# Kernel tuning notes

Hardware: AMD Instinct MI355X
Metric: run time of the kernel (lower is better)

## Reference

```python
import jax, jax.numpy as jnp
import numpy as np

EMB = 1024
N_HEAD = 16
D_K = EMB // N_HEAD


def setup_inputs() -> dict:
    key = jax.random.key(0)
    ks = jax.random.split(key, 11)
    B, S = 4, 2048
    scale = 1.0 / np.sqrt(EMB)
    inp = {
        "q": jax.random.normal(ks[0], (B, S, EMB), jnp.float32),
        "k": jax.random.normal(ks[1], (B, S, EMB), jnp.float32),
        "v": jax.random.normal(ks[2], (B, S, EMB), jnp.float32),
        "Wq": jax.random.normal(ks[3], (EMB, EMB), jnp.float32) * scale,
        "bq": jnp.zeros((EMB,), jnp.float32),
        "Wk": jax.random.normal(ks[4], (EMB, EMB), jnp.float32) * scale,
        "bk": jnp.zeros((EMB,), jnp.float32),
        "Wv": jax.random.normal(ks[5], (EMB, EMB), jnp.float32) * scale,
        "bv": jnp.zeros((EMB,), jnp.float32),
        "Wo": jax.random.normal(ks[6], (EMB, EMB), jnp.float32) * scale,
        "bo": jnp.zeros((EMB,), jnp.float32),
    }
    return inp


def reference(q, k, v, Wq, bq, Wk, bk, Wv, bv, Wo, bo):
    B, S, _ = q.shape
    # project and split heads: [B, H, S, d_k]
    def split(x, W, b):
        y = x @ W.T + b
        return y.reshape(B, -1, N_HEAD, D_K).transpose(0, 2, 1, 3)

    qh = split(q, Wq, bq)
    kh = split(k, Wk, bk)
    vh = split(v, Wv, bv)
    scores = jnp.einsum("bhqd,bhkd->bhqk", qh, kh) / jnp.sqrt(
        jnp.asarray(D_K, qh.dtype))
    attn = jax.nn.softmax(scores, axis=-1)
    out = jnp.einsum("bhqk,bhkd->bhqd", attn, vh)
    out = out.transpose(0, 2, 1, 3).reshape(B, -1, EMB)
    return out @ Wo.T + bo
```

## Files before the change

### kernel.cpp

```cpp
#include <hip/hip_runtime.h>
#include <hip/hip_bf16.h>

#define S_LEN 2048
#define EMB_D 1024
#define NH 16
#define DK 64
#define BATCH 4

typedef __attribute__((ext_vector_type(8))) short short8;
typedef __attribute__((ext_vector_type(4))) float f32x4;
typedef __attribute__((ext_vector_type(8))) unsigned short ushort8;
typedef __attribute__((ext_vector_type(4))) unsigned short ushort4v;
typedef __attribute__((ext_vector_type(4))) unsigned int uint4v;
typedef __attribute__((ext_vector_type(2))) unsigned int uint2v;

__device__ inline unsigned short f2bf(float x) {
    unsigned u = __builtin_bit_cast(unsigned, x);
    u = (u + 0x7fffu + ((u >> 16) & 1u)) >> 16;
    return (unsigned short)u;
}

__device__ inline unsigned cvtpk(float lo, float hi) {
    unsigned r;
    asm("v_cvt_pk_bf16_f32 %0, %1, %2" : "=v"(r) : "v"(lo), "v"(hi));
    return r;
}

typedef const __attribute__((address_space(1))) unsigned int* gas_p;
typedef __attribute__((address_space(3))) unsigned int* las_p;
__device__ inline void gload16(const void* g, void* l) {
    __builtin_amdgcn_global_load_lds((gas_p)g, (las_p)l, 16, 0, 0);
}

struct CvtArgs {
    const float* src[7];
    unsigned short* dst[7];
    int starts[8];
    int ntens;
};

__global__ __launch_bounds__(256) void cvt_all(CvtArgs a) {
    int b = blockIdx.x;
    int t = 0;
#pragma unroll
    for (int i = 1; i < 7; ++i)
        if (i < a.ntens && b >= a.starts[i]) t = i;
    int rel = b - a.starts[t];
    size_t i = (size_t)rel * 2048 + (size_t)threadIdx.x * 8;
    float4 x = *(const float4*)&a.src[t][i];
    float4 y = *(const float4*)&a.src[t][i + 4];
    uint4v w;
    w.x = cvtpk(x.x, x.y); w.y = cvtpk(x.z, x.w);
    w.z = cvtpk(y.x, y.y); w.w = cvtpk(y.z, y.w);
    *(uint4v*)&a.dst[t][i] = w;
}

__global__ __launch_bounds__(256) void gemm_qkv(
    const unsigned short* __restrict__ Aq, const unsigned short* __restrict__ Ak,
    const unsigned short* __restrict__ Av, const unsigned short* __restrict__ Wcat,
    const float* __restrict__ bq, const float* __restrict__ bk, const float* __restrict__ bv,
    unsigned short* __restrict__ Qh, unsigned short* __restrict__ Kh,
    unsigned short* __restrict__ Vt, float qscale)
{
    const int K = EMB_D;
    __shared__ unsigned short As[2][128][64];
    __shared__ unsigned short Bs[2][128][64];

    const int tid = threadIdx.x;
    const int lane = tid & 63;
    const int wid = tid >> 6;
    const int wr = wid >> 1, wc = wid & 1;
    const int l15 = lane & 15, l4 = lane >> 4;
    const int lx7 = l15 & 7;

    const int bid = blockIdx.x;
    const int xcd = bid & 7, j = bid >> 3;
    const int tau = j >> 6, jj = j & 63;
    const int bnl = jj & 7;
    const int bm = xcd * 8 + (jj >> 3);

    const unsigned short* Ab = tau == 0 ? Aq : (tau == 1 ? Ak : Av);
    const unsigned short* Bw = Wcat + (size_t)tau * EMB_D * EMB_D;
    const float* bias = tau == 0 ? bq : (tau == 1 ? bk : bv);
    const float osc = tau == 0 ? qscale : 1.0f;

    const int srow = lane >> 3;
    const int sgl = lane & 7;

    f32x4 acc[4][4];
#pragma unroll
    for (int m = 0; m < 4; ++m)
#pragma unroll
        for (int n = 0; n < 4; ++n) {
            f32x4 z = {0.f, 0.f, 0.f, 0.f};
            acc[m][n] = z;
        }

    auto stageB = [&](int c, int kt) {
#pragma unroll
        for (int q2 = 0; q2 < 4; ++q2) {
            int r = wid * 32 + q2 * 8 + srow;
            gload16(&Bw[(size_t)(bnl * 128 + r) * K + kt * 64 + (sgl ^ srow) * 8],
                    &Bs[c][wid * 32 + q2 * 8][0]);
        }
    };
    auto stageA = [&](int c, int kt) {
#pragma unroll
        for (int q2 = 0; q2 < 4; ++q2) {
            int r = wid * 32 + q2 * 8 + srow;
            gload16(&Ab[(size_t)(bm * 128 + r) * K + kt * 64 + (sgl ^ srow) * 8],
                    &As[c][wid * 32 + q2 * 8][0]);
        }
    };

    stageA(0, 0);
    stageB(0, 0);
    __syncthreads();

    for (int kt = 0; kt < K / 64; ++kt) {
        const int c = kt & 1;
        if (kt + 1 < K / 64) {
            stageA(c ^ 1, kt + 1);
            stageB(c ^ 1, kt + 1);
        }
#pragma unroll
        for (int h = 0; h < 2; ++h) {
            short8 af[4], bf[4];
#pragma unroll
            for (int m = 0; m < 4; ++m)
                af[m] = *(const short8*)&As[c][wr * 64 + m * 16 + l15][((h * 4 + l4) ^ lx7) * 8];
#pragma unroll
            for (int n = 0; n < 4; ++n)
                bf[n] = *(const short8*)&Bs[c][wc * 64 + n * 16 + l15][((h * 4 + l4) ^ lx7) * 8];
#pragma unroll
            for (int m = 0; m < 4; ++m)
#pragma unroll
                for (int n = 0; n < 4; ++n)
                    acc[m][n] = __builtin_amdgcn_mfma_f32_16x16x32_bf16(af[m], bf[n], acc[m][n], 0, 0, 0);
        }
        __syncthreads();
    }

#pragma unroll
    for (int m = 0; m < 4; ++m) {
#pragma unroll
        for (int n = 0; n < 4; ++n) {
            int gm0 = bm * 128 + wr * 64 + m * 16 + l4 * 4;
            int gn = bnl * 128 + wc * 64 + n * 16 + l15;
            if (tau == 2) {
                int b = gm0 >> 11, s0 = gm0 & 2047;
                int h = gn >> 6, d = gn & 63;
                ushort4v w;
#pragma unroll
                for (int r = 0; r < 4; ++r)
                    w[r] = f2bf(acc[m][n][r] + bias[gn]);
                *(ushort4v*)&Vt[((size_t)(b * NH + h) * DK + d) * S_LEN + s0] = w;
            } else {
                unsigned short* Out = tau == 0 ? Qh : Kh;
#pragma unroll
                for (int r = 0; r < 4; ++r) {
                    int gm = gm0 + r;
                    float val = (acc[m][n][r] + bias[gn]) * osc;
                    int b = gm >> 11, s = gm & 2047;
                    int h = gn >> 6, d = gn & 63;
                    Out[((size_t)(b * NH + h) * S_LEN + s) * DK + d] = f2bf(val);
                }
            }
        }
    }
}

template<int A_MODE, int OUT_MODE>
__global__ __launch_bounds__(256) void gemm_bt(
    const void* __restrict__ Aptr, const unsigned short* __restrict__ Bw,
    const float* __restrict__ bias, void* __restrict__ Cout, float oscale)
{
    const int K = EMB_D;
    __shared__ unsigned short As[2][128][64];
    __shared__ unsigned short Bs[2][128][64];

    const int tid = threadIdx.x;
    const int lane = tid & 63;
    const int wid = tid >> 6;
    const int wr = wid >> 1, wc = wid & 1;
    const int l15 = lane & 15, l4 = lane >> 4;
    const int lx7 = l15 & 7;

    const int bid = blockIdx.x;
    const int bm = (bid & 7) * 8 + (bid >> 6);
    const int bn = (bid >> 3) & 7;

    const int srow = lane >> 3;
    const int sgl = lane & 7;

    const float* Af = (const float*)Aptr;
    const unsigned short* Ab = (const unsigned short*)Aptr;

    f32x4 acc[4][4];
#pragma unroll
    for (int m = 0; m < 4; ++m)
#pragma unroll
        for (int n = 0; n < 4; ++n) {
            f32x4 z = {0.f, 0.f, 0.f, 0.f};
            acc[m][n] = z;
        }

    float4 areg[8];

    auto stageB = [&](int c, int kt) {
#pragma unroll
        for (int q2 = 0; q2 < 4; ++q2) {
            int r = wid * 32 + q2 * 8 + srow;
            gload16(&Bw[(size_t)(bn * 128 + r) * K + kt * 64 + (sgl ^ srow) * 8],
                    &Bs[c][wid * 32 + q2 * 8][0]);
        }
    };
    auto stageA1 = [&](int c, int kt) {
#pragma unroll
        for (int q2 = 0; q2 < 4; ++q2) {
            int r = wid * 32 + q2 * 8 + srow;
            gload16(&Ab[(size_t)(bm * 128 + r) * K + kt * 64 + (sgl ^ srow) * 8],
                    &As[c][wid * 32 + q2 * 8][0]);
        }
    };
    auto loadA0 = [&](int kt) {
#pragma unroll
        for (int j = 0; j < 8; ++j) {
            int f = tid + j * 256;
            int r = f >> 4, c4 = f & 15;
            areg[j] = *(const float4*)&Af[(size_t)(bm * 128 + r) * K + kt * 64 + c4 * 4];
        }
    };
    auto writeA0 = [&](int c) {
#pragma unroll
        for (int j = 0; j < 8; ++j) {
            int f = tid + j * 256;
            int r = f >> 4, c4 = f & 15;
            uint2v w;
            w.x = cvtpk(areg[j].x, areg[j].y);
            w.y = cvtpk(areg[j].z, areg[j].w);
            int col = (((c4 >> 1) ^ (r & 7)) << 3) + ((c4 & 1) << 2);
            *(uint2v*)&As[c][r][col] = w;
        }
    };

    if (A_MODE == 0) loadA0(0); else stageA1(0, 0);
    stageB(0, 0);
    if (A_MODE == 0) {
        asm volatile("s_waitcnt vmcnt(0)" ::: "memory");
        writeA0(0);
    }
    __syncthreads();

    for (int kt = 0; kt < K / 64; ++kt) {
        const int c = kt & 1;
        const bool pf = (kt + 1 < K / 64);
        if (pf) {
            if (A_MODE == 0) loadA0(kt + 1); else stageA1(c ^ 1, kt + 1);
            stageB(c ^ 1, kt + 1);
        }
#pragma unroll
        for (int h = 0; h < 2; ++h) {
            short8 af[4], bf[4];
#pragma unroll
            for (int m = 0; m < 4; ++m)
                af[m] = *(const short8*)&As[c][wr * 64 + m * 16 + l15][((h * 4 + l4) ^ lx7) * 8];
#pragma unroll
            for (int n = 0; n < 4; ++n)
                bf[n] = *(const short8*)&Bs[c][wc * 64 + n * 16 + l15][((h * 4 + l4) ^ lx7) * 8];
#pragma unroll
            for (int m = 0; m < 4; ++m)
#pragma unroll
                for (int n = 0; n < 4; ++n)
                    acc[m][n] = __builtin_amdgcn_mfma_f32_16x16x32_bf16(af[m], bf[n], acc[m][n], 0, 0, 0);
        }
        if (pf && A_MODE == 0) {
            asm volatile("s_waitcnt vmcnt(0)" ::: "memory");
            writeA0(c ^ 1);
        }
        __syncthreads();
    }

#pragma unroll
    for (int m = 0; m < 4; ++m) {
#pragma unroll
        for (int n = 0; n < 4; ++n) {
            int gm0 = bm * 128 + wr * 64 + m * 16 + l4 * 4;
            int gn = bn * 128 + wc * 64 + n * 16 + l15;
            if (OUT_MODE == 2) {
                int b = gm0 >> 11, s0 = gm0 & 2047;
                int h = gn >> 6, d = gn & 63;
                ushort4v w;
#pragma unroll
                for (int r = 0; r < 4; ++r)
                    w[r] = f2bf((acc[m][n][r] + bias[gn]) * oscale);
                *(ushort4v*)&((unsigned short*)Cout)[((size_t)(b * NH + h) * DK + d) * S_LEN + s0] = w;
            } else {
#pragma unroll
                for (int r = 0; r < 4; ++r) {
                    int gm = gm0 + r;
                    float val = (acc[m][n][r] + bias[gn]) * oscale;
                    if (OUT_MODE == 1) {
                        int b = gm >> 11, s = gm & 2047;
                        int h = gn >> 6, d = gn & 63;
                        ((unsigned short*)Cout)[((size_t)(b * NH + h) * S_LEN + s) * DK + d] = f2bf(val);
                    } else {
                        ((float*)Cout)[(size_t)gm * EMB_D + gn] = val;
                    }
                }
            }
        }
    }
}

__global__ __launch_bounds__(256, 4) void attn_fwd(
    const unsigned short* __restrict__ Qh, const unsigned short* __restrict__ Kh,
    const unsigned short* __restrict__ Vt, unsigned short* __restrict__ Aout)
{
    __shared__ unsigned short Ks[2][64][64];
    __shared__ unsigned short Vts[2][64][64];

    const int tid = threadIdx.x;
    const int lane = tid & 63;
    const int wid = tid >> 6;
    const int l15 = lane & 15, l4 = lane >> 4;
    const int lx7 = l15 & 7;

    const int bid = blockIdx.x;
    const int swz = (bid & 7) * 128 + (bid >> 3);
    const int bh = swz >> 4, qt = swz & 15;

    const unsigned short* Qb = Qh + (size_t)bh * S_LEN * DK;
    const unsigned short* Kb = Kh + (size_t)bh * S_LEN * DK;
    const unsigned short* Vtb = Vt + (size_t)bh * DK * S_LEN;

    const int srow = lane >> 3;
    const int sgl = lane & 7;

    auto stage = [&](int c, int kt) {
#pragma unroll
        for (int q2 = 0; q2 < 2; ++q2) {
            int q = wid * 2 + q2;
            int rho = q * 8 + srow;
            int kappa = ((rho >> 5) & 1) * 32 + ((rho >> 3) & 1) * 16 +
                        ((rho >> 2) & 1) * 8 + ((rho >> 4) & 1) * 4 + (rho & 3);
            gload16(&Kb[(size_t)(kt * 64 + kappa) * DK + (sgl ^ srow) * 8],
                    &Ks[c][q * 8][0]);
            gload16(&Vtb[(size_t)rho * S_LEN + kt * 64 + (sgl ^ srow) * 8],
                    &Vts[c][q * 8][0]);
        }
    };

    short8 qf[2][2];
#pragma unroll
    for (int m = 0; m < 2; ++m) {
        int qrow = qt * 128 + wid * 32 + m * 16 + l15;
#pragma unroll
        for (int h = 0; h < 2; ++h)
            qf[m][h] = *(const short8*)&Qb[(size_t)qrow * DK + h * 32 + l4 * 8];
    }

    f32x4 ot[2][5];
#pragma unroll
    for (int m = 0; m < 2; ++m)
#pragma unroll
        for (int n = 0; n < 5; ++n) {
            f32x4 z = {0.f, 0.f, 0.f, 0.f};
            ot[m][n] = z;
        }

    short8 ones;
#pragma unroll
    for (int e = 0; e < 8; ++e) ones[e] = (short)0x3F80;

    stage(0, 0);
    __syncthreads();

    for (int kt = 0; kt < S_LEN / 64; ++kt) {
        const int c = kt & 1;
        if (kt + 1 < S_LEN / 64) stage(c ^ 1, kt + 1);

        f32x4 st[2][4];
#pragma unroll
        for (int m = 0; m < 2; ++m)
#pragma unroll
            for (int kb = 0; kb < 4; ++kb) {
                f32x4 z = {0.f, 0.f, 0.f, 0.f};
                st[m][kb] = z;
            }
        __builtin_amdgcn_s_setprio(1);
#pragma unroll
        for (int h = 0; h < 2; ++h)
#pragma unroll
            for (int kb = 0; kb < 4; ++kb) {
                short8 kf = *(const short8*)&Ks[c][kb * 16 + l15][((h * 4 + l4) ^ lx7) * 8];
#pragma unroll
                for (int m = 0; m < 2; ++m)
                    st[m][kb] = __builtin_amdgcn_mfma_f32_16x16x32_bf16(kf, qf[m][h], st[m][kb], 0, 0, 0);
            }
        __builtin_amdgcn_s_setprio(0);

        short8 pa[2][2];
#pragma unroll
        for (int m = 0; m < 2; ++m) {
#pragma unroll
            for (int kb = 0; kb < 4; ++kb)
#pragma unroll
                for (int r = 0; r < 4; ++r)
                    st[m][kb][r] = __builtin_amdgcn_exp2f(st[m][kb][r]);
#pragma unroll
            for (int h = 0; h < 2; ++h) {
                uint4v w;
                w.x = cvtpk(st[m][2 * h][0], st[m][2 * h][1]);
                w.y = cvtpk(st[m][2 * h][2], st[m][2 * h][3]);
                w.z = cvtpk(st[m][2 * h + 1][0], st[m][2 * h + 1][1]);
                w.w = cvtpk(st[m][2 * h + 1][2], st[m][2 * h + 1][3]);
                pa[m][h] = __builtin_bit_cast(short8, w);
            }
        }

        __builtin_amdgcn_s_setprio(1);
#pragma unroll
        for (int n = 0; n < 4; ++n)
#pragma unroll
            for (int h = 0; h < 2; ++h) {
                short8 vb = *(const short8*)&Vts[c][n * 16 + l15][((h * 4 + l4) ^ lx7) * 8];
#pragma unroll
                for (int m = 0; m < 2; ++m)
                    ot[m][n] = __builtin_amdgcn_mfma_f32_16x16x32_bf16(pa[m][h], vb, ot[m][n], 0, 0, 0);
            }
#pragma unroll
        for (int h = 0; h < 2; ++h)
#pragma unroll
            for (int m = 0; m < 2; ++m)
                ot[m][4] = __builtin_amdgcn_mfma_f32_16x16x32_bf16(pa[m][h], ones, ot[m][4], 0, 0, 0);
        __builtin_amdgcn_s_setprio(0);
        __syncthreads();
    }

    const int b = bh >> 4, hh = bh & 15;
#pragma unroll
    for (int m = 0; m < 2; ++m) {
#pragma unroll
        for (int r = 0; r < 4; ++r) {
            float inv = 1.0f / ot[m][4][r];
            int s = qt * 128 + wid * 32 + m * 16 + l4 * 4 + r;
#pragma unroll
            for (int n = 0; n < 4; ++n) {
                int d = n * 16 + l15;
                Aout[((size_t)(b * S_LEN + s)) * EMB_D + hh * DK + d] = f2bf(ot[m][n][r] * inv);
            }
        }
    }
}

extern "C" void kernel_launch(void* const* d_in, const int* in_sizes, int n_in,
                              void* d_out, int out_size, void* d_ws, size_t ws_size,
                              hipStream_t stream) {
    const float* q  = (const float*)d_in[0];
    const float* k  = (const float*)d_in[1];
    const float* v  = (const float*)d_in[2];
    const float* Wq = (const float*)d_in[3];
    const float* bq = (const float*)d_in[4];
    const float* Wk = (const float*)d_in[5];
    const float* bk = (const float*)d_in[6];
    const float* Wv = (const float*)d_in[7];
    const float* bv = (const float*)d_in[8];
    const float* Wo = (const float*)d_in[9];
    const float* bo = (const float*)d_in[10];

    const size_t seg = (size_t)BATCH * NH * S_LEN * DK;
    const size_t wseg = (size_t)EMB_D * EMB_D;
    unsigned short* Qh = (unsigned short*)d_ws;
    unsigned short* Kh = Qh + seg;
    unsigned short* Vh = Kh + seg;
    unsigned short* Ao = Vh + seg;
    unsigned short* Wqb = Ao + seg;
    unsigned short* Wkb = Wqb + wseg;
    unsigned short* Wvb = Wkb + wseg;
    unsigned short* Wob = Wvb + wseg;
    unsigned short* qb = Wob + wseg;
    unsigned short* kb2 = qb + seg;
    unsigned short* vb2 = kb2 + seg;

    const size_t full_elems = seg * 7 + wseg * 4;
    const bool full = ws_size >= full_elems * 2;

    const float qscale = 0.18033688011112042f;

    const int WBLK = (int)(wseg / 2048);
    const int SBLK = (int)(seg / 2048);

    CvtArgs ca;
    ca.src[0] = Wq;  ca.dst[0] = Wqb;
    ca.src[1] = Wk;  ca.dst[1] = Wkb;
    ca.src[2] = Wv;  ca.dst[2] = Wvb;
    ca.src[3] = Wo;  ca.dst[3] = Wob;
    ca.starts[0] = 0;
    ca.starts[1] = WBLK;
    ca.starts[2] = WBLK * 2;
    ca.starts[3] = WBLK * 3;
    int nb = WBLK * 4;
    if (full) {
        ca.src[4] = q; ca.dst[4] = qb;
        ca.src[5] = k; ca.dst[5] = kb2;
        ca.src[6] = v; ca.dst[6] = vb2;
        ca.starts[4] = nb;
        ca.starts[5] = nb + SBLK;
        ca.starts[6] = nb + SBLK * 2;
        ca.ntens = 7;
        nb += SBLK * 3;
    } else {
        ca.src[4] = ca.src[5] = ca.src[6] = Wq;
        ca.dst[4] = ca.dst[5] = ca.dst[6] = Wqb;
        ca.starts[4] = ca.starts[5] = ca.starts[6] = nb;
        ca.ntens = 4;
    }
    ca.starts[7] = nb;
    cvt_all<<<nb, 256, 0, stream>>>(ca);

    if (full) {
        gemm_qkv<<<1536, 256, 0, stream>>>(qb, kb2, vb2, Wqb, bq, bk, bv,
                                           Qh, Kh, Vh, qscale);
    } else {
        gemm_bt<0, 1><<<512, 256, 0, stream>>>((const void*)q, Wqb, bq, (void*)Qh, qscale);
        gemm_bt<0, 1><<<512, 256, 0, stream>>>((const void*)k, Wkb, bk, (void*)Kh, 1.0f);
        gemm_bt<0, 2><<<512, 256, 0, stream>>>((const void*)v, Wvb, bv, (void*)Vh, 1.0f);
    }

    attn_fwd<<<1024, 256, 0, stream>>>(Qh, Kh, Vh, Ao);

    gemm_bt<1, 0><<<512, 256, 0, stream>>>((const void*)Ao, Wob, bo, d_out, 1.0f);
}
```

Measured before the change: 195.1 us.

## Use triple-buffered K=32 pipeline for QKV and output projection GEMMs

Replaces the double-buffered K=64 LDS loop in the QKV projection GEMM with a three-stage K=32 pipeline that prefetches two tiles ahead, using explicit vmcnt waits and raw barriers with sched_barrier fences. A new XOR swizzle fits the narrower tiles. The output projection now uses a dedicated kernel with the same loop instead of the generic gemm_bt, assuming Ao is bf16. The aim is to hide global-load latency better; the cost is twice as many barriers per K and correctness that depends on the hand-written waitcnt counts.

```diff
diff --git a/kernel.cpp b/kernel.cpp
--- a/kernel.cpp
+++ b/kernel.cpp
@@ -55,7 +55,51 @@
     *(uint4v*)&a.dst[t][i] = w;
 }
 
-__global__ __launch_bounds__(256) void gemm_qkv(
+
+#define GEMM32_LOOP(AB_EXPR, BW_EXPR)                                              \
+    auto stage = [&](int s, int kt) {                                              \
+        _Pragma("unroll")                                                          \
+        for (int j2 = 0; j2 < 2; ++j2) {                                           \
+            int rb = j2 * 64 + w16;                                                \
+            gload16(AB_EXPR, &As[s][rb][0]);                                       \
+        }                                                                          \
+        _Pragma("unroll")                                                          \
+        for (int j2 = 0; j2 < 2; ++j2) {                                           \
+            int rb = j2 * 64 + w16;                                                \
+            gload16(BW_EXPR, &Bs[s][rb][0]);                                       \
+        }                                                                          \
+    };                                                                             \
+    stage(0, 0);                                                                   \
+    stage(1, 1);                                                                   \
+    asm volatile("s_waitcnt vmcnt(4)" ::: "memory");                               \
+    __builtin_amdgcn_sched_barrier(0);                                             \
+    __builtin_amdgcn_s_barrier();                                                  \
+    __builtin_amdgcn_sched_barrier(0);                                             \
+    for (int kt = 0; kt < 32; ++kt) {                                              \
+        const int scur = kt % 3;                                                   \
+        if (kt + 2 < 32) stage((kt + 2) % 3, kt + 2);                              \
+        __builtin_amdgcn_sched_barrier(0);                                         \
+        short8 af[4], bf[4];                                                       \
+        _Pragma("unroll")                                                          \
+        for (int m = 0; m < 4; ++m)                                                \
+            af[m] = *(const short8*)&As[scur][wr * 64 + m * 16 + l15][fsl];        \
+        _Pragma("unroll")                                                          \
+        for (int n = 0; n < 4; ++n)                                                \
+            bf[n] = *(const short8*)&Bs[scur][wc * 64 + n * 16 + l15][fsl];        \
+        _Pragma("unroll")                                                          \
+        for (int m = 0; m < 4; ++m)                                                \
+            _Pragma("unroll")                                                      \
+            for (int n = 0; n < 4; ++n)                                            \
+                acc[m][n] = __builtin_amdgcn_mfma_f32_16x16x32_bf16(               \
+                    af[m], bf[n], acc[m][n], 0, 0, 0);                             \
+        if (kt + 2 < 32) { asm volatile("s_waitcnt vmcnt(4)" ::: "memory"); }      \
+        else             { asm volatile("s_waitcnt vmcnt(0)" ::: "memory"); }      \
+        __builtin_amdgcn_sched_barrier(0);                                         \
+        __builtin_amdgcn_s_barrier();                                              \
+        __builtin_amdgcn_sched_barrier(0);                                         \
+    }
+
+__global__ __launch_bounds__(256) void gemm_qkv32(
     const unsigned short* __restrict__ Aq, const unsigned short* __restrict__ Ak,
     const unsigned short* __restrict__ Av, const unsigned short* __restrict__ Wcat,
     const float* __restrict__ bq, const float* __restrict__ bk, const float* __restrict__ bv,
@@ -63,15 +107,14 @@
     unsigned short* __restrict__ Vt, float qscale)
 {
     const int K = EMB_D;
-    __shared__ unsigned short As[2][128][64];
-    __shared__ unsigned short Bs[2][128][64];
+    __shared__ unsigned short As[3][128][32];
+    __shared__ unsigned short Bs[3][128][32];
 
     const int tid = threadIdx.x;
     const int lane = tid & 63;
     const int wid = tid >> 6;
     const int wr = wid >> 1, wc = wid & 1;
     const int l15 = lane & 15, l4 = lane >> 4;
-    const int lx7 = l15 & 7;
 
     const int bid = blockIdx.x;
     const int xcd = bid & 7, j = bid >> 3;
@@ -80,12 +123,14 @@
     const int bm = xcd * 8 + (jj >> 3);
 
     const unsigned short* Ab = tau == 0 ? Aq : (tau == 1 ? Ak : Av);
-    const unsigned short* Bw = Wcat + (size_t)tau * EMB_D * EMB_D;
+    const unsigned short* Bw = Wcat + (size_t)tau * (size_t)EMB_D * EMB_D;
     const float* bias = tau == 0 ? bq : (tau == 1 ? bk : bv);
     const float osc = tau == 0 ? qscale : 1.0f;
 
-    const int srow = lane >> 3;
-    const int sgl = lane & 7;
+    const int srow4 = lane >> 2;
+    const int sgl4 = ((lane & 3) ^ ((lane >> 3) & 3)) * 8;
+    const int w16 = wid * 16;
+    const int fsl = (l4 ^ ((l15 >> 1) & 3)) * 8;
 
     f32x4 acc[4][4];
 #pragma unroll
@@ -96,50 +141,9 @@
             acc[m][n] = z;
         }
 
-    auto stageB = [&](int c, int kt) {
-#pragma unroll
-        for (int q2 = 0; q2 < 4; ++q2) {
-            int r = wid * 32 + q2 * 8 + srow;
-            gload16(&Bw[(size_t)(bnl * 128 + r) * K + kt * 64 + (sgl ^ srow) * 8],
-                    &Bs[c][wid * 32 + q2 * 8][0]);
-        }
-    };
-    auto stageA = [&](int c, int kt) {
-#pragma unroll
-        for (int q2 = 0; q2 < 4; ++q2) {
-            int r = wid * 32 + q2 * 8 + srow;
-            gload16(&Ab[(size_t)(bm * 128 + r) * K + kt * 64 + (sgl ^ srow) * 8],
-                    &As[c][wid * 32 + q2 * 8][0]);
-        }
-    };
-
-    stageA(0, 0);
-    stageB(0, 0);
-    __syncthreads();
-
-    for (int kt = 0; kt < K / 64; ++kt) {
-        const int c = kt & 1;
-        if (kt + 1 < K / 64) {
-            stageA(c ^ 1, kt + 1);
-            stageB(c ^ 1, kt + 1);
-        }
-#pragma unroll
-        for (int h = 0; h < 2; ++h) {
-            short8 af[4], bf[4];
-#pragma unroll
-            for (int m = 0; m < 4; ++m)
-                af[m] = *(const short8*)&As[c][wr * 64 + m * 16 + l15][((h * 4 + l4) ^ lx7) * 8];
-#pragma unroll
-            for (int n = 0; n < 4; ++n)
-                bf[n] = *(const short8*)&Bs[c][wc * 64 + n * 16 + l15][((h * 4 + l4) ^ lx7) * 8];
-#pragma unroll
-            for (int m = 0; m < 4; ++m)
-#pragma unroll
-                for (int n = 0; n < 4; ++n)
-                    acc[m][n] = __builtin_amdgcn_mfma_f32_16x16x32_bf16(af[m], bf[n], acc[m][n], 0, 0, 0);
-        }
-        __syncthreads();
-    }
+    GEMM32_LOOP(
+        &Ab[(size_t)(bm * 128 + rb + srow4) * K + kt * 32 + sgl4],
+        &Bw[(size_t)(bnl * 128 + rb + srow4) * K + kt * 32 + sgl4])
 
 #pragma unroll
     for (int m = 0; m < 4; ++m) {
@@ -166,6 +170,58 @@
                     Out[((size_t)(b * NH + h) * S_LEN + s) * DK + d] = f2bf(val);
                 }
             }
+        }
+    }
+}
+
+__global__ __launch_bounds__(256) void gemm32_f32out(
+    const unsigned short* __restrict__ Ain, const unsigned short* __restrict__ Bwp,
+    const float* __restrict__ bias, float* __restrict__ Cout)
+{
+    const int K = EMB_D;
+    __shared__ unsigned short As[3][128][32];
+    __shared__ unsigned short Bs[3][128][32];
+
+    const int tid = threadIdx.x;
+    const int lane = tid & 63;
+    const int wid = tid >> 6;
+    const int wr = wid >> 1, wc = wid & 1;
+    const int l15 = lane & 15, l4 = lane >> 4;
+
+    const int bid = blockIdx.x;
+    const int bm = (bid & 7) * 8 + (bid >> 6);
+    const int bn = (bid >> 3) & 7;
+
+    const unsigned short* Ab = Ain;
+    const unsigned short* Bw = Bwp;
+
+    const int srow4 = lane >> 2;
+    const int sgl4 = ((lane & 3) ^ ((lane >> 3) & 3)) * 8;
+    const int w16 = wid * 16;
+    const int fsl = (l4 ^ ((l15 >> 1) & 3)) * 8;
+
+    f32x4 acc[4][4];
+#pragma unroll
+    for (int m = 0; m < 4; ++m)
+#pragma unroll
+        for (int n = 0; n < 4; ++n) {
+            f32x4 z = {0.f, 0.f, 0.f, 0.f};
+            acc[m][n] = z;
+        }
+
+    GEMM32_LOOP(
+        &Ab[(size_t)(bm * 128 + rb + srow4) * K + kt * 32 + sgl4],
+        &Bw[(size_t)(bn * 128 + rb + srow4) * K + kt * 32 + sgl4])
+
+#pragma unroll
+    for (int m = 0; m < 4; ++m) {
+#pragma unroll
+        for (int n = 0; n < 4; ++n) {
+            int gm0 = bm * 128 + wr * 64 + m * 16 + l4 * 4;
+            int gn = bn * 128 + wc * 64 + n * 16 + l15;
+#pragma unroll
+            for (int r = 0; r < 4; ++r)
+                Cout[(size_t)(gm0 + r) * EMB_D + gn] = acc[m][n][r] + bias[gn];
         }
     }
 }
@@ -520,8 +576,8 @@
     cvt_all<<<nb, 256, 0, stream>>>(ca);
 
     if (full) {
-        gemm_qkv<<<1536, 256, 0, stream>>>(qb, kb2, vb2, Wqb, bq, bk, bv,
-                                           Qh, Kh, Vh, qscale);
+        gemm_qkv32<<<1536, 256, 0, stream>>>(qb, kb2, vb2, Wqb, bq, bk, bv,
+                                             Qh, Kh, Vh, qscale);
     } else {
         gemm_bt<0, 1><<<512, 256, 0, stream>>>((const void*)q, Wqb, bq, (void*)Qh, qscale);
         gemm_bt<0, 1><<<512, 256, 0, stream>>>((const void*)k, Wkb, bk, (void*)Kh, 1.0f);
@@ -530,5 +586,5 @@
 
     attn_fwd<<<1024, 256, 0, stream>>>(Qh, Kh, Vh, Ao);
 
-    gemm_bt<1, 0><<<512, 256, 0, stream>>>((const void*)Ao, Wob, bo, d_out, 1.0f);
-}
+    gemm32_f32out<<<512, 256, 0, stream>>>(Ao, Wob, bo, (float*)d_out);
+}
```

Measured after the change: 205.6 us. 1.05x slower.

## Single-buffer GEMM LDS tiles for occupancy and add dedicated output-projection kernel

Applied to the files above, without the earlier changes.

The QKV projection GEMM drops its double-buffered LDS staging in favour of a single buffer with a sync after loading, and gains a launch-bounds hint of 4 blocks per CU. The point is to cut LDS and register use so more blocks can be resident and hide latency through occupancy rather than software prefetch. A new gemm_o kernel with the same single-buffer structure and an XCD-aware block mapping replaces the templated gemm_bt for the output projection. The cost is that global loads no longer overlap MFMA work inside a block, and there is an extra barrier every K step.

```diff
diff --git a/kernel.cpp b/kernel.cpp
--- a/kernel.cpp
+++ b/kernel.cpp
@@ -55,7 +55,7 @@
     *(uint4v*)&a.dst[t][i] = w;
 }
 
-__global__ __launch_bounds__(256) void gemm_qkv(
+__global__ __launch_bounds__(256, 4) void gemm_qkv(
     const unsigned short* __restrict__ Aq, const unsigned short* __restrict__ Ak,
     const unsigned short* __restrict__ Av, const unsigned short* __restrict__ Wcat,
     const float* __restrict__ bq, const float* __restrict__ bk, const float* __restrict__ bv,
@@ -63,8 +63,8 @@
     unsigned short* __restrict__ Vt, float qscale)
 {
     const int K = EMB_D;
-    __shared__ unsigned short As[2][128][64];
-    __shared__ unsigned short Bs[2][128][64];
+    __shared__ unsigned short As[128][64];
+    __shared__ unsigned short Bs[128][64];
 
     const int tid = threadIdx.x;
     const int lane = tid & 63;
@@ -80,7 +80,7 @@
     const int bm = xcd * 8 + (jj >> 3);
 
     const unsigned short* Ab = tau == 0 ? Aq : (tau == 1 ? Ak : Av);
-    const unsigned short* Bw = Wcat + (size_t)tau * EMB_D * EMB_D;
+    const unsigned short* Bw = Wcat + (size_t)tau * (size_t)EMB_D * EMB_D;
     const float* bias = tau == 0 ? bq : (tau == 1 ? bk : bv);
     const float osc = tau == 0 ? qscale : 1.0f;
 
@@ -96,42 +96,29 @@
             acc[m][n] = z;
         }
 
-    auto stageB = [&](int c, int kt) {
+    for (int kt = 0; kt < K / 64; ++kt) {
+#pragma unroll
+        for (int q2 = 0; q2 < 4; ++q2) {
+            int r = wid * 32 + q2 * 8 + srow;
+            gload16(&Ab[(size_t)(bm * 128 + r) * K + kt * 64 + (sgl ^ srow) * 8],
+                    &As[wid * 32 + q2 * 8][0]);
+        }
 #pragma unroll
         for (int q2 = 0; q2 < 4; ++q2) {
             int r = wid * 32 + q2 * 8 + srow;
             gload16(&Bw[(size_t)(bnl * 128 + r) * K + kt * 64 + (sgl ^ srow) * 8],
-                    &Bs[c][wid * 32 + q2 * 8][0]);
-        }
-    };
-    auto stageA = [&](int c, int kt) {
-#pragma unroll
-        for (int q2 = 0; q2 < 4; ++q2) {
-            int r = wid * 32 + q2 * 8 + srow;
-            gload16(&Ab[(size_t)(bm * 128 + r) * K + kt * 64 + (sgl ^ srow) * 8],
-                    &As[c][wid * 32 + q2 * 8][0]);
-        }
-    };
-
-    stageA(0, 0);
-    stageB(0, 0);
-    __syncthreads();
-
-    for (int kt = 0; kt < K / 64; ++kt) {
-        const int c = kt & 1;
-        if (kt + 1 < K / 64) {
-            stageA(c ^ 1, kt + 1);
-            stageB(c ^ 1, kt + 1);
-        }
+                    &Bs[wid * 32 + q2 * 8][0]);
+        }
+        __syncthreads();
 #pragma unroll
         for (int h = 0; h < 2; ++h) {
             short8 af[4], bf[4];
 #pragma unroll
             for (int m = 0; m < 4; ++m)
-                af[m] = *(const short8*)&As[c][wr * 64 + m * 16 + l15][((h * 4 + l4) ^ lx7) * 8];
+                af[m] = *(const short8*)&As[wr * 64 + m * 16 + l15][((h * 4 + l4) ^ lx7) * 8];
 #pragma unroll
             for (int n = 0; n < 4; ++n)
-                bf[n] = *(const short8*)&Bs[c][wc * 64 + n * 16 + l15][((h * 4 + l4) ^ lx7) * 8];
+                bf[n] = *(const short8*)&Bs[wc * 64 + n * 16 + l15][((h * 4 + l4) ^ lx7) * 8];
 #pragma unroll
             for (int m = 0; m < 4; ++m)
 #pragma unroll
@@ -166,6 +153,82 @@
                     Out[((size_t)(b * NH + h) * S_LEN + s) * DK + d] = f2bf(val);
                 }
             }
+        }
+    }
+}
+
+__global__ __launch_bounds__(256, 4) void gemm_o(
+    const unsigned short* __restrict__ Ain, const unsigned short* __restrict__ Bw,
+    const float* __restrict__ bias, float* __restrict__ Cout)
+{
+    const int K = EMB_D;
+    __shared__ unsigned short As[128][64];
+    __shared__ unsigned short Bs[128][64];
+
+    const int tid = threadIdx.x;
+    const int lane = tid & 63;
+    const int wid = tid >> 6;
+    const int wr = wid >> 1, wc = wid & 1;
+    const int l15 = lane & 15, l4 = lane >> 4;
+    const int lx7 = l15 & 7;
+
+    const int bid = blockIdx.x;
+    const int bm = (bid & 7) * 8 + (bid >> 6);
+    const int bn = (bid >> 3) & 7;
+
+    const int srow = lane >> 3;
+    const int sgl = lane & 7;
+
+    f32x4 acc[4][4];
+#pragma unroll
+    for (int m = 0; m < 4; ++m)
+#pragma unroll
+        for (int n = 0; n < 4; ++n) {
+            f32x4 z = {0.f, 0.f, 0.f, 0.f};
+            acc[m][n] = z;
+        }
+
+    for (int kt = 0; kt < K / 64; ++kt) {
+#pragma unroll
+        for (int q2 = 0; q2 < 4; ++q2) {
+            int r = wid * 32 + q2 * 8 + srow;
+            gload16(&Ain[(size_t)(bm * 128 + r) * K + kt * 64 + (sgl ^ srow) * 8],
+                    &As[wid * 32 + q2 * 8][0]);
+        }
+#pragma unroll
+        for (int q2 = 0; q2 < 4; ++q2) {
+            int r = wid * 32 + q2 * 8 + srow;
+            gload16(&Bw[(size_t)(bn * 128 + r) * K + kt * 64 + (sgl ^ srow) * 8],
+                    &Bs[wid * 32 + q2 * 8][0]);
+        }
+        __syncthreads();
+#pragma unroll
+        for (int h = 0; h < 2; ++h) {
+            short8 af[4], bf[4];
+#pragma unroll
+            for (int m = 0; m < 4; ++m)
+                af[m] = *(const short8*)&As[wr * 64 + m * 16 + l15][((h * 4 + l4) ^ lx7) * 8];
+#pragma unroll
+            for (int n = 0; n < 4; ++n)
+                bf[n] = *(const short8*)&Bs[wc * 64 + n * 16 + l15][((h * 4 + l4) ^ lx7) * 8];
+#pragma unroll
+            for (int m = 0; m < 4; ++m)
+#pragma unroll
+                for (int n = 0; n < 4; ++n)
+                    acc[m][n] = __builtin_amdgcn_mfma_f32_16x16x32_bf16(af[m], bf[n], acc[m][n], 0, 0, 0);
+        }
+        __syncthreads();
+    }
+
+#pragma unroll
+    for (int m = 0; m < 4; ++m) {
+#pragma unroll
+        for (int n = 0; n < 4; ++n) {
+            int gm0 = bm * 128 + wr * 64 + m * 16 + l4 * 4;
+            int gn = bn * 128 + wc * 64 + n * 16 + l15;
+#pragma unroll
+            for (int r = 0; r < 4; ++r)
+                Cout[(size_t)(gm0 + r) * EMB_D + gn] = acc[m][n][r] + bias[gn];
         }
     }
 }
@@ -530,5 +593,5 @@
 
     attn_fwd<<<1024, 256, 0, stream>>>(Qh, Kh, Vh, Ao);
 
-    gemm_bt<1, 0><<<512, 256, 0, stream>>>((const void*)Ao, Wob, bo, d_out, 1.0f);
-}
+    gemm_o<<<512, 256, 0, stream>>>(Ao, Wob, bo, (float*)d_out);
+}
```

After: 178.6 us (median of 2 runs). 1.09x faster.
